# Optimization experiments

Measured on AMD Instinct MI355X. Metric: run time of the kernel, lower is better.

## Reference

```python
import jax, jax.numpy as jnp
import numpy as np
import math

EPS = 1e-6
N_LAYERS = 4
H = 48
PL = 4 * H  # params per layer (dense variant)
INV = math.log(math.exp(1.0 - EPS) - 1.0)
LOG100 = math.log(100.0)
B, S = 64, 256


def _logc(x):
    # torch: log(x*100)/ - log(100) trick for numerical behavior parity
    return jnp.log(x * 100.0) - LOG100


def _logsig(x):
    # DenseSigmoidFlow uses -softplus(-x) + EPS
    return -jax.nn.softplus(-x) + EPS


def _dense_layer(u_, w_, dsp, x, logdet, in_dim, h):
    # dsp: [B,S,4h], x: [B,in_or_prev_out], logdet: [B,S',out_prev,1] (or [B,1,1,1])
    pre_u = u_[None, None] + dsp[:, :, -in_dim:][:, :, None, :]          # [B,S,h,in]
    pre_w = w_[None, None] + dsp[:, :, 2 * h:3 * h][:, :, None, :]       # [B,S,out,h]
    a = jax.nn.softplus(dsp[:, :, 0:h] + INV) + EPS                       # [B,S,h]
    b = dsp[:, :, h:2 * h]                                                # [B,S,h]
    w = jax.nn.softmax(pre_w, axis=-1)
    u = jax.nn.softmax(pre_u, axis=-1)
    # broadcast-multiply-reduce over in_dim (x broadcasts against u's last dim)
    pre_sigm = jnp.sum(u * a[:, :, :, None] * x[:, None, None, :], axis=-1) + b  # [B,S,h]
    sigm = jax.nn.sigmoid(pre_sigm)
    x_pre = jnp.sum(w * sigm[:, :, None, :], axis=-1)                    # [B,S,out]
    xc = x_pre * (1.0 - EPS) + EPS * 0.5
    xnew = (_logc(xc) - _logc(1.0 - xc))[:, 0, :]                        # [B,out]
    logj = (jax.nn.log_softmax(pre_w, axis=-1)
            + _logsig(pre_sigm)[:, :, None, :]
            + _logsig(-pre_sigm)[:, :, None, :]
            + _logc(a)[:, :, None, :])                                   # [B,S,out,h]
    logj = logj[..., None] + jax.nn.log_softmax(pre_u, axis=-1)[:, :, None, :, :]  # [B,S,out,h,in]
    logj = jax.scipy.special.logsumexp(logj, axis=3)                     # [B,S,out,in]
    logdet_ = logj + math.log(1.0 - EPS) - (_logc(xc) + _logc(1.0 - xc))[:, :, :, None]
    logdet = jax.scipy.special.logsumexp(logdet_[..., None] + logdet[:, :, None, :, :], axis=3)  # [B,S,out,prev]
    return xnew, logdet


def setup_inputs() -> dict:
    key = jax.random.key(0)
    k1, k2, k3, k4, k5, k6 = jax.random.split(key, 6)
    params = jax.random.normal(k1, (B, S, N_LAYERS * PL), dtype=jnp.float32)
    x = jax.random.normal(k2, (B, 1), dtype=jnp.float32)
    lim = 1e-3
    u_mid = jax.random.uniform(k3, (N_LAYERS - 1, H, 1), minval=-lim, maxval=lim, dtype=jnp.float32)
    w_mid = jax.random.uniform(k4, (N_LAYERS - 1, H, H), minval=-lim, maxval=lim, dtype=jnp.float32)
    u_last = jax.random.uniform(k5, (H, H), minval=-lim, maxval=lim, dtype=jnp.float32)
    w_last = jax.random.uniform(k6, (1, H), minval=-lim, maxval=lim, dtype=jnp.float32)
    return {"params": params, "x": x, "u_mid": u_mid, "w_mid": w_mid,
            "u_last": u_last, "w_last": w_last}


def reference(params, x, u_mid, w_mid, u_last, w_last):
    logdet = jnp.zeros((x.shape[0], 1, 1, 1), dtype=x.dtype)
    for i in range(N_LAYERS):
        dsp = params[..., i * PL:(i + 1) * PL]
        if i < N_LAYERS - 1:
            x, logdet = _dense_layer(u_mid[i], w_mid[i], dsp, x, logdet, 1, H)
        else:
            x, logdet = _dense_layer(u_last, w_last, dsp, x, logdet, H, H)
    # final logdet is [B,S,1,1] -> flatten(start_dim=1) -> [B,S]
    return x, logdet.reshape(logdet.shape[0], -1)
```

## Files before the change

kernel.cpp:

```cpp
#include <hip/hip_runtime.h>
#include <math.h>
#include <stdint.h>

#define HH   48
#define RSW  25
#define MATW (HH*RSW)

#define EPSF     1e-6f
#define INVF     0.54132327f
#define LOG1MEPS (-1.0000005e-6f)

static __device__ __forceinline__ float fexp(float x){ return __expf(x); }
static __device__ __forceinline__ float flog(float x){ return __logf(x); }
static __device__ __forceinline__ float frcp(float x){
  float r = __builtin_amdgcn_rcpf(x);
  return r * (2.0f - x * r);
}
static __device__ __forceinline__ float wred_max(float v){
#pragma unroll
  for (int m = 32; m; m >>= 1) v = fmaxf(v, __shfl_xor(v, m, 64));
  return v;
}
static __device__ __forceinline__ float wred_sum(float v){
#pragma unroll
  for (int m = 32; m; m >>= 1) v += __shfl_xor(v, m, 64);
  return v;
}
static __device__ __forceinline__ float fsoftplus(float z){
  return fmaxf(z, 0.0f) + flog(1.0f + fexp(-fabsf(z)));
}
static __device__ __forceinline__ uint32_t bf16_rne(float x){
  uint32_t u = __float_as_uint(x);
  return (u + 0x7fffu + ((u >> 16) & 1u)) >> 16;
}
static __device__ __forceinline__ float bf_lo(uint32_t w){ return __uint_as_float(w << 16); }
static __device__ __forceinline__ float bf_hi(uint32_t w){ return __uint_as_float(w & 0xffff0000u); }

template<int NT>
static __device__ __forceinline__ void init_cmats(uint32_t* CW,
    const float* __restrict__ w_mid, const float* __restrict__ u_last, int tid){
  for (int w = tid; w < 4*HH*24; w += NT){
    int m   = w / (HH*24);
    int rem = w - m*(HH*24);
    int r   = rem / 24, t = rem - r*24;
    const float* src = (m < 3) ? (w_mid + m*HH*HH + r*HH + 2*t)
                               : (u_last + r*HH + 2*t);
    uint32_t b0 = bf16_rne(fexp(src[0]) - 1.0f);
    uint32_t b1 = bf16_rne(fexp(src[1]) - 1.0f);
    CW[m*MATW + r*RSW + t] = b0 | (b1 << 16);
  }
}

#define SIGMOID_FROM_E(ps, E, R) ( ((ps) >= 0.0f) ? (R) : (E)*(R) )

__global__ __launch_bounds__(256) void dsf_xchain(
    const float* __restrict__ params, const float* __restrict__ xin,
    const float* __restrict__ w_mid, const float* __restrict__ u_last,
    const float* __restrict__ w_last, float* __restrict__ ws,
    float* __restrict__ out_x)
{
  __shared__ uint32_t CW[4*MATW];
  __shared__ float4 pk[4][HH];

  init_cmats<256>(CW, w_mid, u_last, threadIdx.x);
  __syncthreads();

  const int wid  = threadIdx.x >> 6;
  const int lane = threadIdx.x & 63;
  const int b    = (blockIdx.x << 2) + wid;
  const bool act = lane < HH;
  const int jj   = act ? lane : (HH-1);
  const float* p = params + (size_t)b * 256 * 768;
  float4* mypk = pk[wid];

  float X  = xin[b];
  float xn = 0.0f;

#pragma unroll
  for (int L = 0; L < 3; ++L){
    const float* q = p + L*192;
    float d0 = q[jj], d1 = q[HH+jj], d2 = q[2*HH+jj];
    float a  = fsoftplus(d0 + INVF) + EPSF;
    float ps = fmaf(a, X, d1);
    float ap = fabsf(ps);
    float E  = fexp(-ap);
    float R  = frcp(1.0f + E);
    float sg = SIGMOID_FROM_E(ps, E, R);
    float e  = act ? fexp(d2) : 0.0f;
    if (act) mypk[lane] = make_float4(e, e*sg, 0.0f, 0.0f);
    __syncthreads();
    float t0 = 0.0f, t1 = 0.0f;
    const uint32_t* Cr = CW + L*MATW + jj*RSW;
#pragma unroll
    for (int t = 0; t < 24; ++t){
      uint32_t cw = Cr[t];
      float c0 = 1.0f + bf_lo(cw), c1 = 1.0f + bf_hi(cw);
      float4 q0 = mypk[2*t], q1 = mypk[2*t+1];
      t0 = fmaf(c0, q0.x, fmaf(c1, q1.x, t0));
      t1 = fmaf(c0, q0.y, fmaf(c1, q1.y, t1));
    }
    __syncthreads();
    float xp = fminf(fmaxf(t1 * frcp(t0), 0.0f), 1.0f);
    float xc = fmaf(xp, 1.0f - EPSF, 0.5f*EPSF);
    xn = flog(xc * frcp(1.0f - xc));
    if (L == 0){ X = wred_sum(act ? xn : 0.0f); if (lane == 0) ws[b] = X; }
    else if (L == 1){ X = wred_sum(act ? xn : 0.0f); if (lane == 0) ws[64 + b] = X; }
    else { if (act) ws[128 + b*HH + lane] = xn; }
  }

  const float* q = p + 3*192;
  float d0 = q[jj], d1 = q[HH+jj], d2 = q[2*HH+jj], d3 = q[3*HH+jj];
  float e3 = act ? fexp(d3) : 0.0f;
  if (act) mypk[lane] = make_float4(e3, e3*xn, 0.0f, 0.0f);
  __syncthreads();
  float s0 = 0.0f, s1 = 0.0f;
  const uint32_t* Ur = CW + 3*MATW + jj*RSW;
#pragma unroll
  for (int t = 0; t < 24; ++t){
    uint32_t cw = Ur[t];
    float c0 = 1.0f + bf_lo(cw), c1 = 1.0f + bf_hi(cw);
    float4 q0 = mypk[2*t], q1 = mypk[2*t+1];
    s0 = fmaf(c0, q0.x, fmaf(c1, q1.x, s0));
    s1 = fmaf(c0, q0.y, fmaf(c1, q1.y, s1));
  }
  float dotx = s1 * frcp(s0);
  float a  = fsoftplus(d0 + INVF) + EPSF;
  float ps = fmaf(a, dotx, d1);
  float ap = fabsf(ps);
  float E  = fexp(-ap);
  float R  = frcp(1.0f + E);
  float sg = SIGMOID_FROM_E(ps, E, R);
  float pw = w_last[jj] + d2;
  float ew = act ? fexp(pw) : 0.0f;
  float Z  = wred_sum(ew);
  float xp = fminf(fmaxf(wred_sum(ew * sg) * frcp(Z), 0.0f), 1.0f);
  float xc = fmaf(xp, 1.0f - EPSF, 0.5f*EPSF);
  if (lane == 0) out_x[b] = flog(xc * frcp(1.0f - xc));
}

__global__ __launch_bounds__(256) void dsf_logdet(
    const float* __restrict__ params, const float* __restrict__ xin,
    const float* __restrict__ w_mid, const float* __restrict__ u_last,
    const float* __restrict__ w_last, const float* __restrict__ ws,
    float* __restrict__ out_ld)
{
  __shared__ uint32_t CW[4*MATW];
  __shared__ float4 pk[4][HH];
  __shared__ float wl[HH];

  init_cmats<256>(CW, w_mid, u_last, threadIdx.x);
  if (threadIdx.x < HH) wl[threadIdx.x] = w_last[threadIdx.x];
  __syncthreads();

  const int wid  = threadIdx.x >> 6;
  const int lane = threadIdx.x & 63;
  const int gw   = (blockIdx.x << 2) + wid;
  const int b    = gw >> 8;
  const bool act = lane < HH;
  const int jj   = act ? lane : (HH-1);
  const float* p = params + (size_t)gw * 768;
  float4* mypk = pk[wid];

  const float Xarr[3] = { xin[b], ws[b], ws[64 + b] };
  float ld = 0.0f;

#pragma unroll
  for (int L = 0; L < 3; ++L){
    const float* q = p + L*192;
    float d0 = q[jj], d1 = q[HH+jj], d2 = q[2*HH+jj];
    float a  = fsoftplus(d0 + INVF) + EPSF;
    float ps = fmaf(a, Xarr[L], d1);
    float ap = fabsf(ps);
    float E  = fexp(-ap);
    float R  = frcp(1.0f + E);
    float sg = SIGMOID_FROM_E(ps, E, R);
    float z  = d2 - ap;
    float M  = wred_max(act ? z : -INFINITY);
    float e  = act ? fexp(d2) : 0.0f;
    float g  = act ? fexp(z - M) * (a * (R * R)) : 0.0f;
    if (act) mypk[lane] = make_float4(e, e*sg, g, 0.0f);
    __syncthreads();
    float t0 = 0.0f, t1 = 0.0f, t2 = 0.0f;
    const uint32_t* Cr = CW + L*MATW + jj*RSW;
#pragma unroll
    for (int t = 0; t < 24; ++t){
      uint32_t cw = Cr[t];
      float c0 = 1.0f + bf_lo(cw), c1 = 1.0f + bf_hi(cw);
      float4 q0 = mypk[2*t], q1 = mypk[2*t+1];
      t0 = fmaf(c0, q0.x, fmaf(c1, q1.x, t0));
      t1 = fmaf(c0, q0.y, fmaf(c1, q1.y, t1));
      t2 = fmaf(c0, q0.z, fmaf(c1, q1.z, t2));
    }
    __syncthreads();
    float xp   = fminf(fmaxf(t1 * frcp(t0), 0.0f), 1.0f);
    float xc   = fmaf(xp, 1.0f - EPSF, 0.5f*EPSF);
    float lsum = flog(xc * (1.0f - xc));
    float lj2  = M + 2.0f*EPSF + flog(t2 * frcp(t0));
    float lsep = 0.0f;
    if (L > 0){
      float mp = wred_max(act ? ld : -INFINITY);
      float sm = wred_sum(act ? fexp(ld - mp) : 0.0f);
      lsep = mp + flog(sm);
    }
    ld = lj2 + LOG1MEPS - lsum + lsep;
  }

  {
    const float* q = p + 3*192;
    float d0 = q[jj], d1 = q[HH+jj], d2 = q[2*HH+jj], d3 = q[3*HH+jj];
    float e3 = act ? fexp(d3) : 0.0f;
    float xv = ws[128 + b*HH + jj];
    if (act) mypk[lane] = make_float4(e3, e3*xv, 0.0f, 0.0f);
    __syncthreads();
    float s0 = 0.0f, s1 = 0.0f;
    const uint32_t* Ur = CW + 3*MATW + jj*RSW;
#pragma unroll
    for (int t = 0; t < 24; ++t){
      uint32_t cw = Ur[t];
      float c0 = 1.0f + bf_lo(cw), c1 = 1.0f + bf_hi(cw);
      float4 q0 = mypk[2*t], q1 = mypk[2*t+1];
      s0 = fmaf(c0, q0.x, fmaf(c1, q1.x, s0));
      s1 = fmaf(c0, q0.y, fmaf(c1, q1.y, s1));
    }
    float dotx = s1 * frcp(s0);
    float lseu = flog(s0);
    float a  = fsoftplus(d0 + INVF) + EPSF;
    float ps = fmaf(a, dotx, d1);
    float ap = fabsf(ps);
    float E  = fexp(-ap);
    float R  = frcp(1.0f + E);
    float sg = SIGMOID_FROM_E(ps, E, R);
    float pw = wl[jj] + d2;
    float ew = act ? fexp(pw) : 0.0f;
    float Z  = wred_sum(ew);
    float xp = fminf(fmaxf(wred_sum(ew * sg) * frcp(Z), 0.0f), 1.0f);
    float lsew = flog(Z);
    float xc   = fmaf(xp, 1.0f - EPSF, 0.5f*EPSF);
    float lsum = flog(xc * (1.0f - xc));
    float y  = pw - ap - lseu;
    float My = wred_max(act ? y : -INFINITY);
    float ec = act ? fexp(y - My) * (a * (R * R)) : 0.0f;
    __syncthreads();
    if (act) mypk[lane].x = ec;
    __syncthreads();
    const uint32_t sh = (jj & 1) ? 0u : 16u;
    const int kw = jj >> 1;
    float acc = 0.0f;
#pragma unroll 8
    for (int j = 0; j < HH; ++j){
      uint32_t cw = CW[3*MATW + j*RSW + kw];
      float cc = 1.0f + __uint_as_float((cw << sh) & 0xffff0000u);
      acc = fmaf(mypk[j].x, cc, acc);
    }
    float lj2k = d3 + My + 2.0f*EPSF - lsew + flog(acc);
    float tot  = act ? (lj2k + LOG1MEPS - lsum + ld) : -INFINITY;
    float Mt = wred_max(tot);
    float sm = wred_sum(act ? fexp(tot - Mt) : 0.0f);
    if (lane == 0) out_ld[gw] = Mt + flog(sm);
  }
}

extern "C" void kernel_launch(void* const* d_in, const int* in_sizes, int n_in,
                              void* d_out, int out_size, void* d_ws, size_t ws_size,
                              hipStream_t stream) {
  const float* params = (const float*)d_in[0];
  const float* xin    = (const float*)d_in[1];
  const float* w_mid  = (const float*)d_in[3];
  const float* u_last = (const float*)d_in[4];
  const float* w_last = (const float*)d_in[5];
  float* out = (float*)d_out;
  float* ws  = (float*)d_ws;

  hipLaunchKernelGGL(dsf_xchain, dim3(16), dim3(256), 0, stream,
                     params, xin, w_mid, u_last, w_last, ws, out);
  hipLaunchKernelGGL(dsf_logdet, dim3(4096), dim3(256), 0, stream,
                     params, xin, w_mid, u_last, w_last, ws, out + 64);
}
```

Before: 169.5 us.

## Replace scalar LDS matvecs in logdet kernel with block-shared bf16 MFMA

```diff
diff --git a/kernel.cpp b/kernel.cpp
--- a/kernel.cpp
+++ b/kernel.cpp
@@ -2,13 +2,17 @@
 #include <math.h>
 #include <stdint.h>
 
-#define HH   48
+#define HH 48
+
 #define RSW  25
 #define MATW (HH*RSW)
 
 #define EPSF     1e-6f
 #define INVF     0.54132327f
 #define LOG1MEPS (-1.0000005e-6f)
+
+typedef float  f32x4  __attribute__((ext_vector_type(4)));
+typedef short  bf16x8 __attribute__((ext_vector_type(8)));
 
 static __device__ __forceinline__ float fexp(float x){ return __expf(x); }
 static __device__ __forceinline__ float flog(float x){ return __logf(x); }
@@ -35,6 +39,11 @@
 }
 static __device__ __forceinline__ float bf_lo(uint32_t w){ return __uint_as_float(w << 16); }
 static __device__ __forceinline__ float bf_hi(uint32_t w){ return __uint_as_float(w & 0xffff0000u); }
+static __device__ __forceinline__ bf16x8 frag_words(uint32_t w0,uint32_t w1,uint32_t w2,uint32_t w3){
+  union { uint32_t w[4]; bf16x8 v; } u; u.w[0]=w0; u.w[1]=w1; u.w[2]=w2; u.w[3]=w3; return u.v;
+}
+
+#define SIGMOID_FROM_E(ps, E, R) ( ((ps) >= 0.0f) ? (R) : (E)*(R) )
 
 template<int NT>
 static __device__ __forceinline__ void init_cmats(uint32_t* CW,
@@ -50,8 +59,6 @@
     CW[m*MATW + r*RSW + t] = b0 | (b1 << 16);
   }
 }
-
-#define SIGMOID_FROM_E(ps, E, R) ( ((ps) >= 0.0f) ? (R) : (E)*(R) )
 
 __global__ __launch_bounds__(256) void dsf_xchain(
     const float* __restrict__ params, const float* __restrict__ xin,
@@ -138,17 +145,43 @@
   if (lane == 0) out_x[b] = flog(xc * frcp(1.0f - xc));
 }
 
+#define AFW (5*3*2*64*4)
+#define PBS 36
+#define TBS 17
+
 __global__ __launch_bounds__(256) void dsf_logdet(
     const float* __restrict__ params, const float* __restrict__ xin,
     const float* __restrict__ w_mid, const float* __restrict__ u_last,
     const float* __restrict__ w_last, const float* __restrict__ ws,
     float* __restrict__ out_ld)
 {
-  __shared__ uint32_t CW[4*MATW];
-  __shared__ float4 pk[4][HH];
+  __shared__ __align__(16) uint32_t AF[AFW];
+  __shared__ __align__(16) uint32_t Pb[16*PBS];
+  __shared__ float Tb[48*TBS];
+  __shared__ float RS[16];
   __shared__ float wl[HH];
 
-  init_cmats<256>(CW, w_mid, u_last, threadIdx.x);
+  for (int idx = threadIdx.x; idx < AFW; idx += 256){
+    int uw   = idx & 3;
+    int lane = (idx >> 2) & 63;
+    int ks   = (idx >> 8) & 1;
+    int mtm  = idx >> 9;
+    int mt   = mtm % 3, mat = mtm / 3;
+    int row  = mt*16 + (lane & 15);
+    int kb   = ks*32 + ((lane >> 4) << 3) + uw*2;
+    float v0 = 0.0f, v1 = 0.0f;
+    if (kb < 48){
+      const float* src;
+      if (mat < 3)      src = w_mid + mat*HH*HH + row*HH;
+      else if (mat == 3) src = u_last + row*HH;
+      else               src = u_last;
+      v0 = (mat == 4) ? fexp(src[kb*HH + row]) - 1.0f : fexp(src[kb]) - 1.0f;
+      if (kb + 1 < 48)
+        v1 = (mat == 4) ? fexp(src[(kb+1)*HH + row]) - 1.0f : fexp(src[kb+1]) - 1.0f;
+    }
+    AF[idx] = bf16_rne(v0) | (bf16_rne(v1) << 16);
+  }
+  for (int idx = threadIdx.x; idx < 16*PBS; idx += 256) Pb[idx] = 0;
   if (threadIdx.x < HH) wl[threadIdx.x] = w_last[threadIdx.x];
   __syncthreads();
 
@@ -159,7 +192,16 @@
   const bool act = lane < HH;
   const int jj   = act ? lane : (HH-1);
   const float* p = params + (size_t)gw * 768;
-  float4* mypk = pk[wid];
+  const int n0   = wid * 3;
+  uint16_t* Pb16 = (uint16_t*)Pb;
+
+  const int colB   = lane & 15;
+  const int kgrp4  = (lane >> 4) << 2;
+  const int rowD0  = (lane >> 4) << 2;
+  const uint32_t onesw = 0x3F803F80u;
+  const bf16x8 onesA0 = frag_words(onesw, onesw, onesw, onesw);
+  const uint32_t hw = (lane < 32) ? onesw : 0u;
+  const bf16x8 onesA1 = frag_words(hw, hw, hw, hw);
 
   const float Xarr[3] = { xin[b], ws[b], ws[64 + b] };
   float ld = 0.0f;
@@ -173,29 +215,51 @@
     float ap = fabsf(ps);
     float E  = fexp(-ap);
     float R  = frcp(1.0f + E);
-    float sg = SIGMOID_FROM_E(ps, E, R);
+    float sg  = SIGMOID_FROM_E(ps, E, R);
+    float sgm = (ps >= 0.0f) ? E*R : R;
     float z  = d2 - ap;
     float M  = wred_max(act ? z : -INFINITY);
-    float e  = act ? fexp(d2) : 0.0f;
-    float g  = act ? fexp(z - M) * (a * (R * R)) : 0.0f;
-    if (act) mypk[lane] = make_float4(e, e*sg, g, 0.0f);
-    __syncthreads();
-    float t0 = 0.0f, t1 = 0.0f, t2 = 0.0f;
-    const uint32_t* Cr = CW + L*MATW + jj*RSW;
-#pragma unroll
-    for (int t = 0; t < 24; ++t){
-      uint32_t cw = Cr[t];
-      float c0 = 1.0f + bf_lo(cw), c1 = 1.0f + bf_hi(cw);
-      float4 q0 = mypk[2*t], q1 = mypk[2*t+1];
-      t0 = fmaf(c0, q0.x, fmaf(c1, q1.x, t0));
-      t1 = fmaf(c0, q0.y, fmaf(c1, q1.y, t1));
-      t2 = fmaf(c0, q0.z, fmaf(c1, q1.z, t2));
-    }
-    __syncthreads();
-    float xp   = fminf(fmaxf(t1 * frcp(t0), 0.0f), 1.0f);
-    float xc   = fmaf(xp, 1.0f - EPSF, 0.5f*EPSF);
-    float lsum = flog(xc * (1.0f - xc));
-    float lj2  = M + 2.0f*EPSF + flog(t2 * frcp(t0));
+    float e  = fexp(d2);
+    float g  = fexp(z - M) * (a * (R * R));
+    if (act){
+      Pb16[(n0+0)*(2*PBS) + jj] = (uint16_t)bf16_rne(e*sg);
+      Pb16[(n0+1)*(2*PBS) + jj] = (uint16_t)bf16_rne(e*sgm);
+      Pb16[(n0+2)*(2*PBS) + jj] = (uint16_t)bf16_rne(g);
+    }
+    __syncthreads();
+    {
+      f32x4 acc = {0.f,0.f,0.f,0.f};
+      const bf16x8 b0 = *(const bf16x8*)&Pb[colB*PBS + kgrp4];
+      const bf16x8 b1 = *(const bf16x8*)&Pb[colB*PBS + 16 + kgrp4];
+      if (wid < 3){
+        const int base = ((L*3 + wid)*2)*256 + lane*4;
+        const bf16x8 a0 = *(const bf16x8*)&AF[base];
+        const bf16x8 a1 = *(const bf16x8*)&AF[base + 256];
+        acc = __builtin_amdgcn_mfma_f32_16x16x32_bf16(a0, b0, acc, 0,0,0);
+        acc = __builtin_amdgcn_mfma_f32_16x16x32_bf16(a1, b1, acc, 0,0,0);
+        const int r0 = wid*16 + rowD0;
+        Tb[(r0+0)*TBS + colB] = acc[0];
+        Tb[(r0+1)*TBS + colB] = acc[1];
+        Tb[(r0+2)*TBS + colB] = acc[2];
+        Tb[(r0+3)*TBS + colB] = acc[3];
+      } else {
+        acc = __builtin_amdgcn_mfma_f32_16x16x32_bf16(onesA0, b0, acc, 0,0,0);
+        acc = __builtin_amdgcn_mfma_f32_16x16x32_bf16(onesA1, b1, acc, 0,0,0);
+        if (lane < 16) RS[lane] = acc[0];
+      }
+    }
+    __syncthreads();
+    float t1  = RS[n0+0] + Tb[jj*TBS + n0+0];
+    float t1m = RS[n0+1] + Tb[jj*TBS + n0+1];
+    float t2  = RS[n0+2] + Tb[jj*TBS + n0+2];
+    float t0  = t1 + t1m;
+    float rt0 = frcp(t0);
+    float xp  = fminf(fmaxf(t1 *rt0, 0.0f), 1.0f);
+    float xpm = fminf(fmaxf(t1m*rt0, 0.0f), 1.0f);
+    float xc  = fmaf(xp , 1.0f - EPSF, 0.5f*EPSF);
+    float xcm = fmaf(xpm, 1.0f - EPSF, 0.5f*EPSF);
+    float lsum = flog(xc * xcm);
+    float lj2  = M + 2.0f*EPSF + flog(t2 * rt0);
     float lsep = 0.0f;
     if (L > 0){
       float mp = wred_max(act ? ld : -INFINITY);
@@ -208,20 +272,37 @@
   {
     const float* q = p + 3*192;
     float d0 = q[jj], d1 = q[HH+jj], d2 = q[2*HH+jj], d3 = q[3*HH+jj];
-    float e3 = act ? fexp(d3) : 0.0f;
+    float e3 = fexp(d3);
     float xv = ws[128 + b*HH + jj];
-    if (act) mypk[lane] = make_float4(e3, e3*xv, 0.0f, 0.0f);
-    __syncthreads();
-    float s0 = 0.0f, s1 = 0.0f;
-    const uint32_t* Ur = CW + 3*MATW + jj*RSW;
-#pragma unroll
-    for (int t = 0; t < 24; ++t){
-      uint32_t cw = Ur[t];
-      float c0 = 1.0f + bf_lo(cw), c1 = 1.0f + bf_hi(cw);
-      float4 q0 = mypk[2*t], q1 = mypk[2*t+1];
-      s0 = fmaf(c0, q0.x, fmaf(c1, q1.x, s0));
-      s1 = fmaf(c0, q0.y, fmaf(c1, q1.y, s1));
-    }
+    if (act){
+      Pb16[(n0+0)*(2*PBS) + jj] = (uint16_t)bf16_rne(e3);
+      Pb16[(n0+1)*(2*PBS) + jj] = (uint16_t)bf16_rne(e3*xv);
+    }
+    __syncthreads();
+    {
+      f32x4 acc = {0.f,0.f,0.f,0.f};
+      const bf16x8 b0 = *(const bf16x8*)&Pb[colB*PBS + kgrp4];
+      const bf16x8 b1 = *(const bf16x8*)&Pb[colB*PBS + 16 + kgrp4];
+      if (wid < 3){
+        const int base = ((3*3 + wid)*2)*256 + lane*4;
+        const bf16x8 a0 = *(const bf16x8*)&AF[base];
+        const bf16x8 a1 = *(const bf16x8*)&AF[base + 256];
+        acc = __builtin_amdgcn_mfma_f32_16x16x32_bf16(a0, b0, acc, 0,0,0);
+        acc = __builtin_amdgcn_mfma_f32_16x16x32_bf16(a1, b1, acc, 0,0,0);
+        const int r0 = wid*16 + rowD0;
+        Tb[(r0+0)*TBS + colB] = acc[0];
+        Tb[(r0+1)*TBS + colB] = acc[1];
+        Tb[(r0+2)*TBS + colB] = acc[2];
+        Tb[(r0+3)*TBS + colB] = acc[3];
+      } else {
+        acc = __builtin_amdgcn_mfma_f32_16x16x32_bf16(onesA0, b0, acc, 0,0,0);
+        acc = __builtin_amdgcn_mfma_f32_16x16x32_bf16(onesA1, b1, acc, 0,0,0);
+        if (lane < 16) RS[lane] = acc[0];
+      }
+    }
+    __syncthreads();
+    float s0 = RS[n0+0] + Tb[jj*TBS + n0+0];
+    float s1 = RS[n0+1] + Tb[jj*TBS + n0+1];
     float dotx = s1 * frcp(s0);
     float lseu = flog(s0);
     float a  = fsoftplus(d0 + INVF) + EPSF;
@@ -229,30 +310,49 @@
     float ap = fabsf(ps);
     float E  = fexp(-ap);
     float R  = frcp(1.0f + E);
-    float sg = SIGMOID_FROM_E(ps, E, R);
+    float sg  = SIGMOID_FROM_E(ps, E, R);
+    float sgm = (ps >= 0.0f) ? E*R : R;
     float pw = wl[jj] + d2;
-    float ew = act ? fexp(pw) : 0.0f;
-    float Z  = wred_sum(ew);
-    float xp = fminf(fmaxf(wred_sum(ew * sg) * frcp(Z), 0.0f), 1.0f);
+    float ew  = act ? fexp(pw) : 0.0f;
+    float Z   = wred_sum(ew);
+    float S1  = wred_sum(ew * sg);
+    float S1m = wred_sum(ew * sgm);
+    float rZ  = frcp(Z);
+    float xp  = fminf(fmaxf(S1 *rZ, 0.0f), 1.0f);
+    float xpm = fminf(fmaxf(S1m*rZ, 0.0f), 1.0f);
     float lsew = flog(Z);
-    float xc   = fmaf(xp, 1.0f - EPSF, 0.5f*EPSF);
-    float lsum = flog(xc * (1.0f - xc));
+    float xc  = fmaf(xp , 1.0f - EPSF, 0.5f*EPSF);
+    float xcm = fmaf(xpm, 1.0f - EPSF, 0.5f*EPSF);
+    float lsum = flog(xc * xcm);
     float y  = pw - ap - lseu;
     float My = wred_max(act ? y : -INFINITY);
-    float ec = act ? fexp(y - My) * (a * (R * R)) : 0.0f;
-    __syncthreads();
-    if (act) mypk[lane].x = ec;
-    __syncthreads();
-    const uint32_t sh = (jj & 1) ? 0u : 16u;
-    const int kw = jj >> 1;
-    float acc = 0.0f;
-#pragma unroll 8
-    for (int j = 0; j < HH; ++j){
-      uint32_t cw = CW[3*MATW + j*RSW + kw];
-      float cc = 1.0f + __uint_as_float((cw << sh) & 0xffff0000u);
-      acc = fmaf(mypk[j].x, cc, acc);
-    }
-    float lj2k = d3 + My + 2.0f*EPSF - lsew + flog(acc);
+    float ec = fexp(y - My) * (a * (R * R));
+    if (act) Pb16[n0*(2*PBS) + jj] = (uint16_t)bf16_rne(ec);
+    __syncthreads();
+    {
+      f32x4 acc = {0.f,0.f,0.f,0.f};
+      const bf16x8 b0 = *(const bf16x8*)&Pb[colB*PBS + kgrp4];
+      const bf16x8 b1 = *(const bf16x8*)&Pb[colB*PBS + 16 + kgrp4];
+      if (wid < 3){
+        const int base = ((4*3 + wid)*2)*256 + lane*4;
+        const bf16x8 a0 = *(const bf16x8*)&AF[base];
+        const bf16x8 a1 = *(const bf16x8*)&AF[base + 256];
+        acc = __builtin_amdgcn_mfma_f32_16x16x32_bf16(a0, b0, acc, 0,0,0);
+        acc = __builtin_amdgcn_mfma_f32_16x16x32_bf16(a1, b1, acc, 0,0,0);
+        const int r0 = wid*16 + rowD0;
+        Tb[(r0+0)*TBS + colB] = acc[0];
+        Tb[(r0+1)*TBS + colB] = acc[1];
+        Tb[(r0+2)*TBS + colB] = acc[2];
+        Tb[(r0+3)*TBS + colB] = acc[3];
+      } else {
+        acc = __builtin_amdgcn_mfma_f32_16x16x32_bf16(onesA0, b0, acc, 0,0,0);
+        acc = __builtin_amdgcn_mfma_f32_16x16x32_bf16(onesA1, b1, acc, 0,0,0);
+        if (lane < 16) RS[lane] = acc[0];
+      }
+    }
+    __syncthreads();
+    float accr = RS[n0] + Tb[jj*TBS + n0];
+    float lj2k = d3 + My + 2.0f*EPSF - lsew + flog(accr);
     float tot  = act ? (lj2k + LOG1MEPS - lsum + ld) : -INFINITY;
     float Mt = wred_max(tot);
     float sm = wred_sum(act ? fexp(tot - Mt) : 0.0f);
```

Result: no change. 166.8 us (-1.6%).
